# Performance work log

Hardware: AMD Instinct MI355X
Metric: run time of the kernel (lower is better)

The kernel has to match this reference:

```python
import jax, jax.numpy as jnp
import numpy as np

N_NODES = 100000
SELF_LOOP_W = 2.0  # improved=True in PyG GCNConv -> self-loop fill value 2.0


def gcn_conv(x, src, dst, ew, W, b, n_nodes):
    """PyG GCNConv (improved=True): x' = D^-1/2 (A + 2I) D^-1/2 (x W) + b."""
    h = x @ W  # [N, out]
    loop = jnp.arange(n_nodes, dtype=src.dtype)
    src_f = jnp.concatenate([src, loop])
    dst_f = jnp.concatenate([dst, loop])
    ew_f = jnp.concatenate([ew, jnp.full((n_nodes,), SELF_LOOP_W, dtype=ew.dtype)])
    deg = jax.ops.segment_sum(ew_f, dst_f, num_segments=n_nodes)  # [N]
    dinv = jnp.where(deg > 0, jax.lax.rsqrt(jnp.where(deg > 0, deg, 1.0)), 0.0)
    norm = dinv[src_f] * ew_f * dinv[dst_f]  # [E+N]
    msg = h[src_f] * norm[:, None]  # [E+N, out]
    out = jax.ops.segment_sum(msg, dst_f, num_segments=n_nodes)
    return out + b


def setup_inputs() -> dict:
    key = jax.random.key(0)
    k1, k2, k3, k4, k5 = jax.random.split(key, 5)
    N, E = N_NODES, 3200000
    F0, F1, F2 = 128, 128, 64
    x = jax.random.normal(k1, (N, F0), dtype=jnp.float32)
    edges = jax.random.randint(k2, (2, E), 0, N, dtype=jnp.int64)
    weights = jax.random.uniform(k3, (E,), dtype=jnp.float32)
    # kaiming_uniform on weight of shape [out, in]; stored transposed for x @ W
    bnd0 = float(np.sqrt(6.0 / F0))
    bnd1 = float(np.sqrt(6.0 / F1))
    W0 = jax.random.uniform(k4, (F0, F1), dtype=jnp.float32, minval=-bnd0, maxval=bnd0)
    W1 = jax.random.uniform(k5, (F1, F2), dtype=jnp.float32, minval=-bnd1, maxval=bnd1)
    b0 = jnp.zeros((F1,), dtype=jnp.float32)
    b1 = jnp.zeros((F2,), dtype=jnp.float32)
    return {"x": x, "edges": edges, "weights": weights,
            "W0": W0, "b0": b0, "W1": W1, "b1": b1}


def reference(x, edges, weights, W0, b0, W1, b1):
    src, dst = edges[0], edges[1]
    n = x.shape[0]
    h = gcn_conv(x, src, dst, weights, W0, b0, n)
    h = jax.nn.relu(h)
    h = gcn_conv(h, src, dst, weights, W1, b1, n)
    return jax.nn.sigmoid(h)
```

## Files before the change

### kernel.cpp

```cpp
#include <hip/hip_runtime.h>
#include <math.h>

typedef __attribute__((ext_vector_type(8))) short bf16x8;
typedef __attribute__((ext_vector_type(4))) float f32x4;


__device__ __forceinline__ unsigned short f2b(float f) {
  unsigned u = __float_as_uint(f);
  unsigned r = u + 0x7fffu + ((u >> 16) & 1u);
  return (unsigned short)(r >> 16);
}
__device__ __forceinline__ float b2f_lo(unsigned v) {
  return __uint_as_float(v << 16);
}
__device__ __forceinline__ float b2f_hi(unsigned v) {
  return __uint_as_float(v & 0xffff0000u);
}


__global__ __launch_bounds__(256) void bucket_hist(const int* __restrict__ dst,
                                                   int* __restrict__ blkhist,
                                                   int NB, int E, int chunk) {
  extern __shared__ int sm_hist[];
  for (int i = threadIdx.x; i < NB; i += 256) sm_hist[i] = 0;
  __syncthreads();
  const int b = blockIdx.x;
  const int beg = b * chunk;
  const int end = min(E, beg + chunk);
  int j = beg + threadIdx.x;
  for (; j + 768 < end; j += 1024) {
    const int d0 = dst[j], d1 = dst[j + 256], d2 = dst[j + 512], d3 = dst[j + 768];
    atomicAdd(&sm_hist[d0 >> 6], 1);
    atomicAdd(&sm_hist[d1 >> 6], 1);
    atomicAdd(&sm_hist[d2 >> 6], 1);
    atomicAdd(&sm_hist[d3 >> 6], 1);
  }
  for (; j < end; j += 256) atomicAdd(&sm_hist[dst[j] >> 6], 1);
  __syncthreads();
  for (int i = threadIdx.x; i < NB; i += 256) blkhist[(long)b * NB + i] = sm_hist[i];
}

__global__ __launch_bounds__(256) void col_prefix(int* __restrict__ blkhist,
                                                  int* __restrict__ btot, int NB,
                                                  int nblk) {
  const int k = blockIdx.x * 256 + threadIdx.x;
  if (k >= NB) return;
  int run = 0;
  int b = 0;
  for (; b + 4 <= nblk; b += 4) {
    const int t0 = blkhist[(long)(b + 0) * NB + k];
    const int t1 = blkhist[(long)(b + 1) * NB + k];
    const int t2 = blkhist[(long)(b + 2) * NB + k];
    const int t3 = blkhist[(long)(b + 3) * NB + k];
    blkhist[(long)(b + 0) * NB + k] = run; run += t0;
    blkhist[(long)(b + 1) * NB + k] = run; run += t1;
    blkhist[(long)(b + 2) * NB + k] = run; run += t2;
    blkhist[(long)(b + 3) * NB + k] = run; run += t3;
  }
  for (; b < nblk; ++b) {
    const int t = blkhist[(long)b * NB + k];
    blkhist[(long)b * NB + k] = run;
    run += t;
  }
  btot[k] = run;
}

__global__ __launch_bounds__(256) void scan_single(int* __restrict__ cr, int n) {
  __shared__ int sm[256];
  __shared__ int sbase;
  if (threadIdx.x == 0) sbase = 0;
  __syncthreads();
  for (int c0 = 0; c0 < n; c0 += 256) {
    const int i = c0 + threadIdx.x;
    const int v = (i < n) ? cr[i] : 0;
    sm[threadIdx.x] = v;
    __syncthreads();
    for (int off = 1; off < 256; off <<= 1) {
      int a = (threadIdx.x >= off) ? sm[threadIdx.x - off] : 0;
      __syncthreads();
      sm[threadIdx.x] += a;
      __syncthreads();
    }
    const int b = sbase;
    const int tot = sm[255];
    if (i < n) cr[i] = b + sm[threadIdx.x] - v;
    __syncthreads();
    if (threadIdx.x == 0) sbase = b + tot;
    __syncthreads();
  }
  if (threadIdx.x == 0) cr[n] = sbase;
}

__global__ __launch_bounds__(256) void bucket_scatter(const int* __restrict__ src,
                                                      const int* __restrict__ dst,
                                                      const float* __restrict__ ew,
                                                      const int* __restrict__ blkhist,
                                                      const int* __restrict__ bstart,
                                                      uint2* __restrict__ bkt, int NB,
                                                      int E, int chunk) {
  extern __shared__ int sm_cur[];
  const int b = blockIdx.x;
  for (int i = threadIdx.x; i < NB; i += 256)
    sm_cur[i] = blkhist[(long)b * NB + i] + bstart[i];
  __syncthreads();
  const int beg = b * chunk;
  const int end = min(E, beg + chunk);
  int j = beg + threadIdx.x;
  for (; j + 768 < end; j += 1024) {
    const int d0 = dst[j], d1 = dst[j + 256], d2 = dst[j + 512], d3 = dst[j + 768];
    const int s0 = src[j], s1 = src[j + 256], s2 = src[j + 512], s3 = src[j + 768];
    const float e0 = ew[j], e1 = ew[j + 256], e2 = ew[j + 512], e3 = ew[j + 768];
    int q0 = (int)(e0 * 32767.f + 0.5f); q0 = (q0 < 0) ? 0 : ((q0 > 32767) ? 32767 : q0);
    int q1 = (int)(e1 * 32767.f + 0.5f); q1 = (q1 < 0) ? 0 : ((q1 > 32767) ? 32767 : q1);
    int q2 = (int)(e2 * 32767.f + 0.5f); q2 = (q2 < 0) ? 0 : ((q2 > 32767) ? 32767 : q2);
    int q3 = (int)(e3 * 32767.f + 0.5f); q3 = (q3 < 0) ? 0 : ((q3 > 32767) ? 32767 : q3);
    const int p0 = atomicAdd(&sm_cur[d0 >> 6], 1);
    bkt[p0] = make_uint2(((unsigned)s0 << 15) | (unsigned)q0, (unsigned)(d0 & 63));
    const int p1 = atomicAdd(&sm_cur[d1 >> 6], 1);
    bkt[p1] = make_uint2(((unsigned)s1 << 15) | (unsigned)q1, (unsigned)(d1 & 63));
    const int p2 = atomicAdd(&sm_cur[d2 >> 6], 1);
    bkt[p2] = make_uint2(((unsigned)s2 << 15) | (unsigned)q2, (unsigned)(d2 & 63));
    const int p3 = atomicAdd(&sm_cur[d3 >> 6], 1);
    bkt[p3] = make_uint2(((unsigned)s3 << 15) | (unsigned)q3, (unsigned)(d3 & 63));
  }
  for (; j < end; j += 256) {
    const int d = dst[j];
    int q = (int)(ew[j] * 32767.f + 0.5f);
    q = (q < 0) ? 0 : ((q > 32767) ? 32767 : q);
    const unsigned rec = ((unsigned)src[j] << 15) | (unsigned)q;
    const int pos = atomicAdd(&sm_cur[d >> 6], 1);
    bkt[pos] = make_uint2(rec, (unsigned)(d & 63));
  }
}

__global__ __launch_bounds__(256) void bucket_finalize(const uint2* __restrict__ bkt,
                                                       const int* __restrict__ bstart,
                                                       unsigned* __restrict__ recs,
                                                       int* __restrict__ row_start,
                                                       float* __restrict__ dinv, int NB,
                                                       int N, int E) {
  __shared__ int hist[64], qs[64], cur[64], lstart[64];
  const int k = blockIdx.x;
  const int t = threadIdx.x;
  if (t < 64) { hist[t] = 0; qs[t] = 0; }
  __syncthreads();
  const int beg = bstart[k], end = bstart[k + 1];
  for (int j = beg + t; j < end; j += 256) {
    const uint2 v = bkt[j];
    atomicAdd(&hist[v.y], 1);
    atomicAdd(&qs[v.y], (int)(v.x & 32767u));
  }
  __syncthreads();
  if (t == 0) {
    int run = 0;
    for (int i = 0; i < 64; ++i) { lstart[i] = run; run += hist[i]; }
  }
  __syncthreads();
  if (t < 64) {
    cur[t] = lstart[t];
    const int node = k * 64 + t;
    if (node < N) {
      row_start[node] = beg + lstart[t];
      dinv[node] = rsqrtf((float)qs[t] * (1.f / 32767.f) + 2.0f);
    }
  }
  if (k == NB - 1 && t == 0) row_start[N] = E;
  __syncthreads();
  for (int j = beg + t; j < end; j += 256) {
    const uint2 v = bkt[j];
    const int off = atomicAdd(&cur[v.y], 1);
    recs[beg + off] = v.x;
  }
}


__global__ __launch_bounds__(256) void fold_dinv(unsigned int* __restrict__ recs,
                                                 const float* __restrict__ dinv, int E) {
  int i = blockIdx.x * 256 + threadIdx.x;
  if (i >= E) return;
  const unsigned rec = recs[i];
  const int s = rec >> 15;
  const float v = (float)(rec & 32767u) * (1.f / 32767.f) * dinv[s];
  int q = (int)(v * (32767.f / 0.75f) + 0.5f);
  q = (q > 32767) ? 32767 : q;
  recs[i] = ((unsigned)s << 15) | (unsigned)q;
}


__global__ __launch_bounds__(256) void to_bf16_8(const float* __restrict__ x,
                                                 unsigned short* __restrict__ xb,
                                                 int n8) {
  int i = blockIdx.x * 256 + threadIdx.x;
  if (i >= n8) return;
  const float4 a = *(const float4*)&x[(long)i * 8];
  const float4 b = *(const float4*)&x[(long)i * 8 + 4];
  uint4 o;
  o.x = (unsigned)f2b(a.x) | ((unsigned)f2b(a.y) << 16);
  o.y = (unsigned)f2b(a.z) | ((unsigned)f2b(a.w) << 16);
  o.z = (unsigned)f2b(b.x) | ((unsigned)f2b(b.y) << 16);
  o.w = (unsigned)f2b(b.z) | ((unsigned)f2b(b.w) << 16);
  *(uint4*)&xb[(long)i * 8] = o;
}

__global__ __launch_bounds__(256) void pack_wfrag(const float* __restrict__ W,
                                                  unsigned short* __restrict__ frag,
                                                  int C, int total) {
  int i = blockIdx.x * 256 + threadIdx.x;
  if (i >= total) return;
  const int e = i & 7;
  const int lane = (i >> 3) & 63;
  const int t = i >> 9;
  const int kk = t & 3;
  const int ct = t >> 2;
  const int k = kk * 32 + (lane >> 4) * 8 + e;
  const int c = ct * 16 + (lane & 15);
  frag[i] = f2b(W[(long)k * C + c]);
}


__global__ __launch_bounds__(256) void gather_l1_half(const uint4* __restrict__ xb4,
                                                      const unsigned int* __restrict__ recs,
                                                      const int* __restrict__ row_start,
                                                      const float* __restrict__ dinv,
                                                      uint4* __restrict__ xab4, int N,
                                                      int half) {
  const int t = blockIdx.x * 256 + threadIdx.x;
  const int d = t >> 3;
  if (d >= N) return;
  const int jl = (t & 7) + half * 8;
  const int beg = row_start[d], end = row_start[d + 1];
  const float dd = dinv[d];
  constexpr float S = 0.75f / 32767.f;
  const uint4 sv = xb4[(long)d * 16 + jl];
  const float sl = 2.f * dd * dd;
  float aca[8], acb[8];
  aca[0] = b2f_lo(sv.x) * sl; aca[1] = b2f_hi(sv.x) * sl;
  aca[2] = b2f_lo(sv.y) * sl; aca[3] = b2f_hi(sv.y) * sl;
  aca[4] = b2f_lo(sv.z) * sl; aca[5] = b2f_hi(sv.z) * sl;
  aca[6] = b2f_lo(sv.w) * sl; aca[7] = b2f_hi(sv.w) * sl;
#pragma unroll
  for (int u = 0; u < 8; ++u) acb[u] = 0.f;
  int j = beg;
  for (; j + 8 <= end; j += 8) {
    unsigned rr[8];
    uint4 vv[8];
#pragma unroll
    for (int u = 0; u < 8; ++u) rr[u] = recs[j + u];
#pragma unroll
    for (int u = 0; u < 8; ++u) vv[u] = xb4[(long)(rr[u] >> 15) * 16 + jl];
#pragma unroll
    for (int u = 0; u < 8; ++u) {
      const float cf = (float)(rr[u] & 32767u) * S * dd;
      float* ac = (u & 1) ? acb : aca;
      ac[0] = fmaf(cf, b2f_lo(vv[u].x), ac[0]);
      ac[1] = fmaf(cf, b2f_hi(vv[u].x), ac[1]);
      ac[2] = fmaf(cf, b2f_lo(vv[u].y), ac[2]);
      ac[3] = fmaf(cf, b2f_hi(vv[u].y), ac[3]);
      ac[4] = fmaf(cf, b2f_lo(vv[u].z), ac[4]);
      ac[5] = fmaf(cf, b2f_hi(vv[u].z), ac[5]);
      ac[6] = fmaf(cf, b2f_lo(vv[u].w), ac[6]);
      ac[7] = fmaf(cf, b2f_hi(vv[u].w), ac[7]);
    }
  }
  for (; j < end; ++j) {
    const unsigned rec = recs[j];
    const uint4 v = xb4[(long)(rec >> 15) * 16 + jl];
    const float cf = (float)(rec & 32767u) * S * dd;
    aca[0] = fmaf(cf, b2f_lo(v.x), aca[0]);
    aca[1] = fmaf(cf, b2f_hi(v.x), aca[1]);
    aca[2] = fmaf(cf, b2f_lo(v.y), aca[2]);
    aca[3] = fmaf(cf, b2f_hi(v.y), aca[3]);
    aca[4] = fmaf(cf, b2f_lo(v.z), aca[4]);
    aca[5] = fmaf(cf, b2f_hi(v.z), aca[5]);
    aca[6] = fmaf(cf, b2f_lo(v.w), aca[6]);
    aca[7] = fmaf(cf, b2f_hi(v.w), aca[7]);
  }
#pragma unroll
  for (int u = 0; u < 8; ++u) aca[u] += acb[u];
  uint4 o;
  o.x = (unsigned)f2b(aca[0]) | ((unsigned)f2b(aca[1]) << 16);
  o.y = (unsigned)f2b(aca[2]) | ((unsigned)f2b(aca[3]) << 16);
  o.z = (unsigned)f2b(aca[4]) | ((unsigned)f2b(aca[5]) << 16);
  o.w = (unsigned)f2b(aca[6]) | ((unsigned)f2b(aca[7]) << 16);
  xab4[(long)d * 16 + jl] = o;
}


__global__ __launch_bounds__(256) void fused_mlp_mfma(
    const unsigned short* __restrict__ xab, const unsigned short* __restrict__ w0f,
    const float* __restrict__ b0, const unsigned short* __restrict__ w1f,
    unsigned short* __restrict__ r2b, int N) {
  __shared__ unsigned short Hl[4][16][136];
  const int tid = threadIdx.x;
  const int w = tid >> 6, l = tid & 63;
  const int lr = l & 15, lg = l >> 4;
  const int row0 = blockIdx.x * 64 + w * 16;

  int arow = row0 + lr;
  if (arow >= N) arow = N - 1;
  const unsigned short* ap = xab + (long)arow * 128 + lg * 8;
  const bf16x8 a0 = *(const bf16x8*)(ap);
  const bf16x8 a1 = *(const bf16x8*)(ap + 32);
  const bf16x8 a2 = *(const bf16x8*)(ap + 64);
  const bf16x8 a3 = *(const bf16x8*)(ap + 96);

  for (int ct = 0; ct < 8; ++ct) {
    const unsigned short* bp = w0f + ct * 2048 + l * 8;
    f32x4 acc = {0.f, 0.f, 0.f, 0.f};
    acc = __builtin_amdgcn_mfma_f32_16x16x32_bf16(a0, *(const bf16x8*)(bp), acc, 0, 0, 0);
    acc = __builtin_amdgcn_mfma_f32_16x16x32_bf16(a1, *(const bf16x8*)(bp + 512), acc, 0, 0, 0);
    acc = __builtin_amdgcn_mfma_f32_16x16x32_bf16(a2, *(const bf16x8*)(bp + 1024), acc, 0, 0, 0);
    acc = __builtin_amdgcn_mfma_f32_16x16x32_bf16(a3, *(const bf16x8*)(bp + 1536), acc, 0, 0, 0);
    const float bv = b0[ct * 16 + lr];
#pragma unroll
    for (int r = 0; r < 4; ++r) {
      Hl[w][lg * 4 + r][ct * 16 + lr] = f2b(fmaxf(acc[r] + bv, 0.f));
    }
  }

  const unsigned short* hp = &Hl[w][lr][lg * 8];
  const bf16x8 h0 = *(const bf16x8*)(hp);
  const bf16x8 h1 = *(const bf16x8*)(hp + 32);
  const bf16x8 h2 = *(const bf16x8*)(hp + 64);
  const bf16x8 h3 = *(const bf16x8*)(hp + 96);

  for (int ct = 0; ct < 4; ++ct) {
    const unsigned short* bp = w1f + ct * 2048 + l * 8;
    f32x4 acc = {0.f, 0.f, 0.f, 0.f};
    acc = __builtin_amdgcn_mfma_f32_16x16x32_bf16(h0, *(const bf16x8*)(bp), acc, 0, 0, 0);
    acc = __builtin_amdgcn_mfma_f32_16x16x32_bf16(h1, *(const bf16x8*)(bp + 512), acc, 0, 0, 0);
    acc = __builtin_amdgcn_mfma_f32_16x16x32_bf16(h2, *(const bf16x8*)(bp + 1024), acc, 0, 0, 0);
    acc = __builtin_amdgcn_mfma_f32_16x16x32_bf16(h3, *(const bf16x8*)(bp + 1536), acc, 0, 0, 0);
#pragma unroll
    for (int r = 0; r < 4; ++r) {
      const int orow = row0 + lg * 4 + r;
      if (orow < N) r2b[(long)orow * 64 + ct * 16 + lr] = f2b(acc[r]);
    }
  }
}


__global__ __launch_bounds__(256) void gather_l2(const uint4* __restrict__ r2b4,
                                                 const unsigned int* __restrict__ recs,
                                                 const int* __restrict__ row_start,
                                                 const float* __restrict__ dinv,
                                                 const float* __restrict__ b1,
                                                 float* __restrict__ out, int N) {
  const int t = blockIdx.x * 256 + threadIdx.x;
  const int d = t >> 3;
  if (d >= N) return;
  const int jl = t & 7;
  const int beg = row_start[d], end = row_start[d + 1];
  const float dd = dinv[d];
  constexpr float S = 0.75f / 32767.f;
  const uint4 sv = r2b4[(long)d * 8 + jl];
  const float sl = 2.f * dd * dd;
  float aca[8], acb[8];
  aca[0] = b2f_lo(sv.x) * sl; aca[1] = b2f_hi(sv.x) * sl;
  aca[2] = b2f_lo(sv.y) * sl; aca[3] = b2f_hi(sv.y) * sl;
  aca[4] = b2f_lo(sv.z) * sl; aca[5] = b2f_hi(sv.z) * sl;
  aca[6] = b2f_lo(sv.w) * sl; aca[7] = b2f_hi(sv.w) * sl;
#pragma unroll
  for (int u = 0; u < 8; ++u) acb[u] = 0.f;
  int j = beg;
  for (; j + 8 <= end; j += 8) {
    unsigned rr[8];
    uint4 vv[8];
#pragma unroll
    for (int u = 0; u < 8; ++u) rr[u] = recs[j + u];
#pragma unroll
    for (int u = 0; u < 8; ++u) vv[u] = r2b4[(long)(rr[u] >> 15) * 8 + jl];
#pragma unroll
    for (int u = 0; u < 8; ++u) {
      const float cf = (float)(rr[u] & 32767u) * S * dd;
      float* ac = (u & 1) ? acb : aca;
      ac[0] = fmaf(cf, b2f_lo(vv[u].x), ac[0]);
      ac[1] = fmaf(cf, b2f_hi(vv[u].x), ac[1]);
      ac[2] = fmaf(cf, b2f_lo(vv[u].y), ac[2]);
      ac[3] = fmaf(cf, b2f_hi(vv[u].y), ac[3]);
      ac[4] = fmaf(cf, b2f_lo(vv[u].z), ac[4]);
      ac[5] = fmaf(cf, b2f_hi(vv[u].z), ac[5]);
      ac[6] = fmaf(cf, b2f_lo(vv[u].w), ac[6]);
      ac[7] = fmaf(cf, b2f_hi(vv[u].w), ac[7]);
    }
  }
  for (; j < end; ++j) {
    const unsigned rec = recs[j];
    const uint4 v = r2b4[(long)(rec >> 15) * 8 + jl];
    const float cf = (float)(rec & 32767u) * S * dd;
    aca[0] = fmaf(cf, b2f_lo(v.x), aca[0]);
    aca[1] = fmaf(cf, b2f_hi(v.x), aca[1]);
    aca[2] = fmaf(cf, b2f_lo(v.y), aca[2]);
    aca[3] = fmaf(cf, b2f_hi(v.y), aca[3]);
    aca[4] = fmaf(cf, b2f_lo(v.z), aca[4]);
    aca[5] = fmaf(cf, b2f_hi(v.z), aca[5]);
    aca[6] = fmaf(cf, b2f_lo(v.w), aca[6]);
    aca[7] = fmaf(cf, b2f_hi(v.w), aca[7]);
  }
#pragma unroll
  for (int u = 0; u < 8; ++u) aca[u] += acb[u];
  const int c = jl * 8;
  const float4 ba = *(const float4*)&b1[c];
  const float4 bb = *(const float4*)&b1[c + 4];
  float4 o1, o2;
  o1.x = 1.f / (1.f + __expf(-(aca[0] + ba.x)));
  o1.y = 1.f / (1.f + __expf(-(aca[1] + ba.y)));
  o1.z = 1.f / (1.f + __expf(-(aca[2] + ba.z)));
  o1.w = 1.f / (1.f + __expf(-(aca[3] + ba.w)));
  o2.x = 1.f / (1.f + __expf(-(aca[4] + bb.x)));
  o2.y = 1.f / (1.f + __expf(-(aca[5] + bb.y)));
  o2.z = 1.f / (1.f + __expf(-(aca[6] + bb.z)));
  o2.w = 1.f / (1.f + __expf(-(aca[7] + bb.w)));
  *(float4*)&out[(long)d * 64 + c] = o1;
  *(float4*)&out[(long)d * 64 + c + 4] = o2;
}


extern "C" void kernel_launch(void* const* d_in, const int* in_sizes, int n_in,
                              void* d_out, int out_size, void* d_ws, size_t ws_size,
                              hipStream_t stream) {
  const float* x  = (const float*)d_in[0];
  const int* src  = (const int*)d_in[1];
  const float* ew = (const float*)d_in[2];
  const float* W0 = (const float*)d_in[3];
  const float* b0 = (const float*)d_in[4];
  const float* W1 = (const float*)d_in[5];
  const float* b1 = (const float*)d_in[6];
  float* out = (float*)d_out;

  const int N = in_sizes[0] / 128;
  const int E = in_sizes[2];
  const int* dstp = src + E;

  const int NB = (N + 63) >> 6;
  const int NBLK = 1024;
  const int chunk = (E + NBLK - 1) / NBLK;

  float* ws = (float*)d_ws;
  const size_t oN = ((size_t)N + 255) & ~(size_t)255;
  float* dinv = ws;
  int* rowst = (int*)(ws + oN);
  int* bstart = rowst + oN;
  int* bsum = bstart + 2048;
  int* blkhist = bsum + 1024;
  unsigned int* recs = (unsigned int*)(blkhist + (size_t)NBLK * NB);
  unsigned int* xb = recs + E;
  uint2* bkt = (uint2*)xb;
  const size_t xb_units = ((size_t)2 * E > (size_t)N * 64) ? (size_t)2 * E : (size_t)N * 64;
  unsigned int* xab = xb + xb_units;
  unsigned short* w0f = (unsigned short*)(xab + (size_t)N * 64);
  unsigned short* w1f = w0f + 16384;
  unsigned int* r2b = xb;

  const int nbE = (E + 255) / 256;
  const int nblkB = (NB + 255) / 256;

  bucket_hist<<<NBLK, 256, NB * 4, stream>>>(dstp, blkhist, NB, E, chunk);
  col_prefix<<<nblkB, 256, 0, stream>>>(blkhist, bstart, NB, NBLK);
  scan_single<<<1, 256, 0, stream>>>(bstart, NB);
  bucket_scatter<<<NBLK, 256, NB * 4, stream>>>(src, dstp, ew, blkhist, bstart, bkt, NB,
                                                E, chunk);
  bucket_finalize<<<NB, 256, 0, stream>>>(bkt, bstart, recs, rowst, dinv, NB, N, E);
  fold_dinv<<<nbE, 256, 0, stream>>>(recs, dinv, E);

  pack_wfrag<<<64, 256, 0, stream>>>(W0, w0f, 128, 16384);
  pack_wfrag<<<32, 256, 0, stream>>>(W1, w1f, 64, 8192);
  to_bf16_8<<<(N * 16 + 255) / 256, 256, 0, stream>>>(x, (unsigned short*)xb, N * 16);

  const int gl1b = (N * 8 + 255) / 256;
  gather_l1_half<<<gl1b, 256, 0, stream>>>((const uint4*)xb, recs, rowst, dinv,
                                           (uint4*)xab, N, 0);
  gather_l1_half<<<gl1b, 256, 0, stream>>>((const uint4*)xb, recs, rowst, dinv,
                                           (uint4*)xab, N, 1);

  fused_mlp_mfma<<<(N + 63) / 64, 256, 0, stream>>>((const unsigned short*)xab, w0f, b0,
                                                    w1f, (unsigned short*)r2b, N);
  gather_l2<<<(N * 8 + 255) / 256, 256, 0, stream>>>((const uint4*)r2b, recs, rowst, dinv,
                                                     b1, out, N);
}
```

Baseline: 385.2 us.

## Split gathers into narrow column passes and parallelize bucket column prefix

The feature gathers for both layers now run as several launches, each covering only two 16-byte column slices per node: eight passes for layer 1 and four for layer 2. The goal is a smaller gathered working set per pass so it stays cache resident, at the cost of re-reading the edge records and row offsets in every pass. The bucket column prefix becomes a three-stage partial-sum, scan and apply over 16 groups, and the histogram block count doubles to 2048, with blkhist moved into the xab region. The paired-accumulator ILP in the gathers is removed, which lengthens each FMA dependency chain.

```diff
diff --git a/kernel.cpp b/kernel.cpp
--- a/kernel.cpp
+++ b/kernel.cpp
@@ -3,6 +3,10 @@
 
 typedef __attribute__((ext_vector_type(8))) short bf16x8;
 typedef __attribute__((ext_vector_type(4))) float f32x4;
+
+#define NBLK 2048
+#define GB   16
+#define BPG  (NBLK / GB)
 
 
 __device__ __forceinline__ unsigned short f2b(float f) {
@@ -40,29 +44,63 @@
   for (int i = threadIdx.x; i < NB; i += 256) blkhist[(long)b * NB + i] = sm_hist[i];
 }
 
-__global__ __launch_bounds__(256) void col_prefix(int* __restrict__ blkhist,
-                                                  int* __restrict__ btot, int NB,
-                                                  int nblk) {
+__global__ __launch_bounds__(256) void col_part(const int* __restrict__ blkhist,
+                                                int* __restrict__ partials, int NB) {
+  const int k = blockIdx.x * 256 + threadIdx.x;
+  const int g = blockIdx.y;
+  if (k >= NB) return;
+  const long base = (long)g * BPG * NB + k;
+  int sum = 0;
+  int i = 0;
+  for (; i + 4 <= BPG; i += 4) {
+    const int t0 = blkhist[base + (long)(i + 0) * NB];
+    const int t1 = blkhist[base + (long)(i + 1) * NB];
+    const int t2 = blkhist[base + (long)(i + 2) * NB];
+    const int t3 = blkhist[base + (long)(i + 3) * NB];
+    sum += t0 + t1 + t2 + t3;
+  }
+  for (; i < BPG; ++i) sum += blkhist[base + (long)i * NB];
+  partials[(long)g * NB + k] = sum;
+}
+
+__global__ __launch_bounds__(256) void col_scan16(int* __restrict__ partials,
+                                                  int* __restrict__ bstart, int NB) {
   const int k = blockIdx.x * 256 + threadIdx.x;
   if (k >= NB) return;
   int run = 0;
-  int b = 0;
-  for (; b + 4 <= nblk; b += 4) {
-    const int t0 = blkhist[(long)(b + 0) * NB + k];
-    const int t1 = blkhist[(long)(b + 1) * NB + k];
-    const int t2 = blkhist[(long)(b + 2) * NB + k];
-    const int t3 = blkhist[(long)(b + 3) * NB + k];
-    blkhist[(long)(b + 0) * NB + k] = run; run += t0;
-    blkhist[(long)(b + 1) * NB + k] = run; run += t1;
-    blkhist[(long)(b + 2) * NB + k] = run; run += t2;
-    blkhist[(long)(b + 3) * NB + k] = run; run += t3;
-  }
-  for (; b < nblk; ++b) {
-    const int t = blkhist[(long)b * NB + k];
-    blkhist[(long)b * NB + k] = run;
+#pragma unroll
+  for (int g = 0; g < GB; ++g) {
+    const int t = partials[(long)g * NB + k];
+    partials[(long)g * NB + k] = run;
     run += t;
   }
-  btot[k] = run;
+  bstart[k] = run;
+}
+
+__global__ __launch_bounds__(256) void col_apply(int* __restrict__ blkhist,
+                                                 const int* __restrict__ partials,
+                                                 int NB) {
+  const int k = blockIdx.x * 256 + threadIdx.x;
+  const int g = blockIdx.y;
+  if (k >= NB) return;
+  const long base = (long)g * BPG * NB + k;
+  int run = partials[(long)g * NB + k];
+  int i = 0;
+  for (; i + 4 <= BPG; i += 4) {
+    const int t0 = blkhist[base + (long)(i + 0) * NB];
+    const int t1 = blkhist[base + (long)(i + 1) * NB];
+    const int t2 = blkhist[base + (long)(i + 2) * NB];
+    const int t3 = blkhist[base + (long)(i + 3) * NB];
+    blkhist[base + (long)(i + 0) * NB] = run; run += t0;
+    blkhist[base + (long)(i + 1) * NB] = run; run += t1;
+    blkhist[base + (long)(i + 2) * NB] = run; run += t2;
+    blkhist[base + (long)(i + 3) * NB] = run; run += t3;
+  }
+  for (; i < BPG; ++i) {
+    const int t = blkhist[base + (long)i * NB];
+    blkhist[base + (long)i * NB] = run;
+    run += t;
+  }
 }
 
 __global__ __launch_bounds__(256) void scan_single(int* __restrict__ cr, int n) {
@@ -218,28 +256,26 @@
 }
 
 
-__global__ __launch_bounds__(256) void gather_l1_half(const uint4* __restrict__ xb4,
+__global__ __launch_bounds__(256) void gather_l1_pass(const uint4* __restrict__ xb4,
                                                       const unsigned int* __restrict__ recs,
                                                       const int* __restrict__ row_start,
                                                       const float* __restrict__ dinv,
                                                       uint4* __restrict__ xab4, int N,
-                                                      int half) {
+                                                      int slot) {
   const int t = blockIdx.x * 256 + threadIdx.x;
-  const int d = t >> 3;
+  const int d = t >> 1;
   if (d >= N) return;
-  const int jl = (t & 7) + half * 8;
+  const int jl = slot + (t & 1);
   const int beg = row_start[d], end = row_start[d + 1];
   const float dd = dinv[d];
   constexpr float S = 0.75f / 32767.f;
   const uint4 sv = xb4[(long)d * 16 + jl];
   const float sl = 2.f * dd * dd;
-  float aca[8], acb[8];
-  aca[0] = b2f_lo(sv.x) * sl; aca[1] = b2f_hi(sv.x) * sl;
-  aca[2] = b2f_lo(sv.y) * sl; aca[3] = b2f_hi(sv.y) * sl;
-  aca[4] = b2f_lo(sv.z) * sl; aca[5] = b2f_hi(sv.z) * sl;
-  aca[6] = b2f_lo(sv.w) * sl; aca[7] = b2f_hi(sv.w) * sl;
-#pragma unroll
-  for (int u = 0; u < 8; ++u) acb[u] = 0.f;
+  float acc[8];
+  acc[0] = b2f_lo(sv.x) * sl; acc[1] = b2f_hi(sv.x) * sl;
+  acc[2] = b2f_lo(sv.y) * sl; acc[3] = b2f_hi(sv.y) * sl;
+  acc[4] = b2f_lo(sv.z) * sl; acc[5] = b2f_hi(sv.z) * sl;
+  acc[6] = b2f_lo(sv.w) * sl; acc[7] = b2f_hi(sv.w) * sl;
   int j = beg;
   for (; j + 8 <= end; j += 8) {
     unsigned rr[8];
@@ -251,37 +287,34 @@
 #pragma unroll
     for (int u = 0; u < 8; ++u) {
       const float cf = (float)(rr[u] & 32767u) * S * dd;
-      float* ac = (u & 1) ? acb : aca;
-      ac[0] = fmaf(cf, b2f_lo(vv[u].x), ac[0]);
-      ac[1] = fmaf(cf, b2f_hi(vv[u].x), ac[1]);
-      ac[2] = fmaf(cf, b2f_lo(vv[u].y), ac[2]);
-      ac[3] = fmaf(cf, b2f_hi(vv[u].y), ac[3]);
-      ac[4] = fmaf(cf, b2f_lo(vv[u].z), ac[4]);
-      ac[5] = fmaf(cf, b2f_hi(vv[u].z), ac[5]);
-      ac[6] = fmaf(cf, b2f_lo(vv[u].w), ac[6]);
-      ac[7] = fmaf(cf, b2f_hi(vv[u].w), ac[7]);
+      acc[0] = fmaf(cf, b2f_lo(vv[u].x), acc[0]);
+      acc[1] = fmaf(cf, b2f_hi(vv[u].x), acc[1]);
+      acc[2] = fmaf(cf, b2f_lo(vv[u].y), acc[2]);
+      acc[3] = fmaf(cf, b2f_hi(vv[u].y), acc[3]);
+      acc[4] = fmaf(cf, b2f_lo(vv[u].z), acc[4]);
+      acc[5] = fmaf(cf, b2f_hi(vv[u].z), acc[5]);
+      acc[6] = fmaf(cf, b2f_lo(vv[u].w), acc[6]);
+      acc[7] = fmaf(cf, b2f_hi(vv[u].w), acc[7]);
     }
   }
   for (; j < end; ++j) {
     const unsigned rec = recs[j];
     const uint4 v = xb4[(long)(rec >> 15) * 16 + jl];
     const float cf = (float)(rec & 32767u) * S * dd;
-    aca[0] = fmaf(cf, b2f_lo(v.x), aca[0]);
-    aca[1] = fmaf(cf, b2f_hi(v.x), aca[1]);
-    aca[2] = fmaf(cf, b2f_lo(v.y), aca[2]);
-    aca[3] = fmaf(cf, b2f_hi(v.y), aca[3]);
-    aca[4] = fmaf(cf, b2f_lo(v.z), aca[4]);
-    aca[5] = fmaf(cf, b2f_hi(v.z), aca[5]);
-    aca[6] = fmaf(cf, b2f_lo(v.w), aca[6]);
-    aca[7] = fmaf(cf, b2f_hi(v.w), aca[7]);
-  }
-#pragma unroll
-  for (int u = 0; u < 8; ++u) aca[u] += acb[u];
+    acc[0] = fmaf(cf, b2f_lo(v.x), acc[0]);
+    acc[1] = fmaf(cf, b2f_hi(v.x), acc[1]);
+    acc[2] = fmaf(cf, b2f_lo(v.y), acc[2]);
+    acc[3] = fmaf(cf, b2f_hi(v.y), acc[3]);
+    acc[4] = fmaf(cf, b2f_lo(v.z), acc[4]);
+    acc[5] = fmaf(cf, b2f_hi(v.z), acc[5]);
+    acc[6] = fmaf(cf, b2f_lo(v.w), acc[6]);
+    acc[7] = fmaf(cf, b2f_hi(v.w), acc[7]);
+  }
   uint4 o;
-  o.x = (unsigned)f2b(aca[0]) | ((unsigned)f2b(aca[1]) << 16);
-  o.y = (unsigned)f2b(aca[2]) | ((unsigned)f2b(aca[3]) << 16);
-  o.z = (unsigned)f2b(aca[4]) | ((unsigned)f2b(aca[5]) << 16);
-  o.w = (unsigned)f2b(aca[6]) | ((unsigned)f2b(aca[7]) << 16);
+  o.x = (unsigned)f2b(acc[0]) | ((unsigned)f2b(acc[1]) << 16);
+  o.y = (unsigned)f2b(acc[2]) | ((unsigned)f2b(acc[3]) << 16);
+  o.z = (unsigned)f2b(acc[4]) | ((unsigned)f2b(acc[5]) << 16);
+  o.w = (unsigned)f2b(acc[6]) | ((unsigned)f2b(acc[7]) << 16);
   xab4[(long)d * 16 + jl] = o;
 }
 
@@ -340,28 +373,27 @@
 }
 
 
-__global__ __launch_bounds__(256) void gather_l2(const uint4* __restrict__ r2b4,
-                                                 const unsigned int* __restrict__ recs,
-                                                 const int* __restrict__ row_start,
-                                                 const float* __restrict__ dinv,
-                                                 const float* __restrict__ b1,
-                                                 float* __restrict__ out, int N) {
+__global__ __launch_bounds__(256) void gather_l2_pass(const uint4* __restrict__ r2b4,
+                                                      const unsigned int* __restrict__ recs,
+                                                      const int* __restrict__ row_start,
+                                                      const float* __restrict__ dinv,
+                                                      const float* __restrict__ b1,
+                                                      float* __restrict__ out, int N,
+                                                      int slot) {
   const int t = blockIdx.x * 256 + threadIdx.x;
-  const int d = t >> 3;
+  const int d = t >> 1;
   if (d >= N) return;
-  const int jl = t & 7;
+  const int jl = slot + (t & 1);
   const int beg = row_start[d], end = row_start[d + 1];
   const float dd = dinv[d];
   constexpr float S = 0.75f / 32767.f;
   const uint4 sv = r2b4[(long)d * 8 + jl];
   const float sl = 2.f * dd * dd;
-  float aca[8], acb[8];
-  aca[0] = b2f_lo(sv.x) * sl; aca[1] = b2f_hi(sv.x) * sl;
-  aca[2] = b2f_lo(sv.y) * sl; aca[3] = b2f_hi(sv.y) * sl;
-  aca[4] = b2f_lo(sv.z) * sl; aca[5] = b2f_hi(sv.z) * sl;
-  aca[6] = b2f_lo(sv.w) * sl; aca[7] = b2f_hi(sv.w) * sl;
-#pragma unroll
-  for (int u = 0; u < 8; ++u) acb[u] = 0.f;
+  float acc[8];
+  acc[0] = b2f_lo(sv.x) * sl; acc[1] = b2f_hi(sv.x) * sl;
+  acc[2] = b2f_lo(sv.y) * sl; acc[3] = b2f_hi(sv.y) * sl;
+  acc[4] = b2f_lo(sv.z) * sl; acc[5] = b2f_hi(sv.z) * sl;
+  acc[6] = b2f_lo(sv.w) * sl; acc[7] = b2f_hi(sv.w) * sl;
   int j = beg;
   for (; j + 8 <= end; j += 8) {
     unsigned rr[8];
@@ -373,44 +405,41 @@
 #pragma unroll
     for (int u = 0; u < 8; ++u) {
       const float cf = (float)(rr[u] & 32767u) * S * dd;
-      float* ac = (u & 1) ? acb : aca;
-      ac[0] = fmaf(cf, b2f_lo(vv[u].x), ac[0]);
-      ac[1] = fmaf(cf, b2f_hi(vv[u].x), ac[1]);
-      ac[2] = fmaf(cf, b2f_lo(vv[u].y), ac[2]);
-      ac[3] = fmaf(cf, b2f_hi(vv[u].y), ac[3]);
-      ac[4] = fmaf(cf, b2f_lo(vv[u].z), ac[4]);
-      ac[5] = fmaf(cf, b2f_hi(vv[u].z), ac[5]);
-      ac[6] = fmaf(cf, b2f_lo(vv[u].w), ac[6]);
-      ac[7] = fmaf(cf, b2f_hi(vv[u].w), ac[7]);
+      acc[0] = fmaf(cf, b2f_lo(vv[u].x), acc[0]);
+      acc[1] = fmaf(cf, b2f_hi(vv[u].x), acc[1]);
+      acc[2] = fmaf(cf, b2f_lo(vv[u].y), acc[2]);
+      acc[3] = fmaf(cf, b2f_hi(vv[u].y), acc[3]);
+      acc[4] = fmaf(cf, b2f_lo(vv[u].z), acc[4]);
+      acc[5] = fmaf(cf, b2f_hi(vv[u].z), acc[5]);
+      acc[6] = fmaf(cf, b2f_lo(vv[u].w), acc[6]);
+      acc[7] = fmaf(cf, b2f_hi(vv[u].w), acc[7]);
     }
   }
   for (; j < end; ++j) {
     const unsigned rec = recs[j];
     const uint4 v = r2b4[(long)(rec >> 15) * 8 + jl];
     const float cf = (float)(rec & 32767u) * S * dd;
-    aca[0] = fmaf(cf, b2f_lo(v.x), aca[0]);
-    aca[1] = fmaf(cf, b2f_hi(v.x), aca[1]);
-    aca[2] = fmaf(cf, b2f_lo(v.y), aca[2]);
-    aca[3] = fmaf(cf, b2f_hi(v.y), aca[3]);
-    aca[4] = fmaf(cf, b2f_lo(v.z), aca[4]);
-    aca[5] = fmaf(cf, b2f_hi(v.z), aca[5]);
-    aca[6] = fmaf(cf, b2f_lo(v.w), aca[6]);
-    aca[7] = fmaf(cf, b2f_hi(v.w), aca[7]);
-  }
-#pragma unroll
-  for (int u = 0; u < 8; ++u) aca[u] += acb[u];
+    acc[0] = fmaf(cf, b2f_lo(v.x), acc[0]);
+    acc[1] = fmaf(cf, b2f_hi(v.x), acc[1]);
+    acc[2] = fmaf(cf, b2f_lo(v.y), acc[2]);
+    acc[3] = fmaf(cf, b2f_hi(v.y), acc[3]);
+    acc[4] = fmaf(cf, b2f_lo(v.z), acc[4]);
+    acc[5] = fmaf(cf, b2f_hi(v.z), acc[5]);
+    acc[6] = fmaf(cf, b2f_lo(v.w), acc[6]);
+    acc[7] = fmaf(cf, b2f_hi(v.w), acc[7]);
+  }
   const int c = jl * 8;
   const float4 ba = *(const float4*)&b1[c];
   const float4 bb = *(const float4*)&b1[c + 4];
   float4 o1, o2;
-  o1.x = 1.f / (1.f + __expf(-(aca[0] + ba.x)));
-  o1.y = 1.f / (1.f + __expf(-(aca[1] + ba.y)));
-  o1.z = 1.f / (1.f + __expf(-(aca[2] + ba.z)));
-  o1.w = 1.f / (1.f + __expf(-(aca[3] + ba.w)));
-  o2.x = 1.f / (1.f + __expf(-(aca[4] + bb.x)));
-  o2.y = 1.f / (1.f + __expf(-(aca[5] + bb.y)));
-  o2.z = 1.f / (1.f + __expf(-(aca[6] + bb.z)));
-  o2.w = 1.f / (1.f + __expf(-(aca[7] + bb.w)));
+  o1.x = 1.f / (1.f + __expf(-(acc[0] + ba.x)));
+  o1.y = 1.f / (1.f + __expf(-(acc[1] + ba.y)));
+  o1.z = 1.f / (1.f + __expf(-(acc[2] + ba.z)));
+  o1.w = 1.f / (1.f + __expf(-(acc[3] + ba.w)));
+  o2.x = 1.f / (1.f + __expf(-(acc[4] + bb.x)));
+  o2.y = 1.f / (1.f + __expf(-(acc[5] + bb.y)));
+  o2.z = 1.f / (1.f + __expf(-(acc[6] + bb.z)));
+  o2.w = 1.f / (1.f + __expf(-(acc[7] + bb.w)));
   *(float4*)&out[(long)d * 64 + c] = o1;
   *(float4*)&out[(long)d * 64 + c + 4] = o2;
 }
@@ -433,7 +462,6 @@
   const int* dstp = src + E;
 
   const int NB = (N + 63) >> 6;
-  const int NBLK = 1024;
   const int chunk = (E + NBLK - 1) / NBLK;
 
   float* ws = (float*)d_ws;
@@ -441,13 +469,13 @@
   float* dinv = ws;
   int* rowst = (int*)(ws + oN);
   int* bstart = rowst + oN;
-  int* bsum = bstart + 2048;
-  int* blkhist = bsum + 1024;
-  unsigned int* recs = (unsigned int*)(blkhist + (size_t)NBLK * NB);
+  int* partials = bstart + 2048;
+  unsigned int* recs = (unsigned int*)(partials + 32768);
   unsigned int* xb = recs + E;
   uint2* bkt = (uint2*)xb;
   const size_t xb_units = ((size_t)2 * E > (size_t)N * 64) ? (size_t)2 * E : (size_t)N * 64;
   unsigned int* xab = xb + xb_units;
+  int* blkhist = (int*)xab;
   unsigned short* w0f = (unsigned short*)(xab + (size_t)N * 64);
   unsigned short* w1f = w0f + 16384;
   unsigned int* r2b = xb;
@@ -456,7 +484,9 @@
   const int nblkB = (NB + 255) / 256;
 
   bucket_hist<<<NBLK, 256, NB * 4, stream>>>(dstp, blkhist, NB, E, chunk);
-  col_prefix<<<nblkB, 256, 0, stream>>>(blkhist, bstart, NB, NBLK);
+  col_part<<<dim3(nblkB, GB), 256, 0, stream>>>(blkhist, partials, NB);
+  col_scan16<<<nblkB, 256, 0, stream>>>(partials, bstart, NB);
+  col_apply<<<dim3(nblkB, GB), 256, 0, stream>>>(blkhist, partials, NB);
   scan_single<<<1, 256, 0, stream>>>(bstart, NB);
   bucket_scatter<<<NBLK, 256, NB * 4, stream>>>(src, dstp, ew, blkhist, bstart, bkt, NB,
                                                 E, chunk);
@@ -467,14 +497,15 @@
   pack_wfrag<<<32, 256, 0, stream>>>(W1, w1f, 64, 8192);
   to_bf16_8<<<(N * 16 + 255) / 256, 256, 0, stream>>>(x, (unsigned short*)xb, N * 16);
 
-  const int gl1b = (N * 8 + 255) / 256;
-  gather_l1_half<<<gl1b, 256, 0, stream>>>((const uint4*)xb, recs, rowst, dinv,
-                                           (uint4*)xab, N, 0);
-  gather_l1_half<<<gl1b, 256, 0, stream>>>((const uint4*)xb, recs, rowst, dinv,
-                                           (uint4*)xab, N, 1);
+  const int gpb = (N * 2 + 255) / 256;
+  for (int p = 0; p < 8; ++p)
+    gather_l1_pass<<<gpb, 256, 0, stream>>>((const uint4*)xb, recs, rowst, dinv,
+                                            (uint4*)xab, N, p * 2);
 
   fused_mlp_mfma<<<(N + 63) / 64, 256, 0, stream>>>((const unsigned short*)xab, w0f, b0,
                                                     w1f, (unsigned short*)r2b, N);
-  gather_l2<<<(N * 8 + 255) / 256, 256, 0, stream>>>((const uint4*)r2b, recs, rowst, dinv,
-                                                     b1, out, N);
-}
+
+  for (int p = 0; p < 4; ++p)
+    gather_l2_pass<<<gpb, 256, 0, stream>>>((const uint4*)r2b, recs, rowst, dinv, b1,
+                                            out, N, p * 2);
+}
```

Measured after the change: 844.0 us. 119% more time.

## Widen destination buckets to 256 nodes and parallelize column prefix scan

Applied to the files above, without the earlier changes.

Destination buckets now cover 256 nodes instead of 64, which cuts the bucket count and therefore the size of the per-block histogram matrix and the shared-memory histograms. The serial per-column prefix over 1024 blocks is split into three kernels: a grouped partial sum, a 16-way scan of the partials, and an apply pass, so many more threads take part. The blkhist buffer moves to reuse the xab region. The trade-off is more kernel launches and fewer, larger finalize blocks with a longer serial local scan over 256 entries.

```diff
diff --git a/kernel.cpp b/kernel.cpp
--- a/kernel.cpp
+++ b/kernel.cpp
@@ -3,6 +3,10 @@
 
 typedef __attribute__((ext_vector_type(8))) short bf16x8;
 typedef __attribute__((ext_vector_type(4))) float f32x4;
+
+#define NBLK 1024
+#define GB   16
+#define BPG  (NBLK / GB)
 
 
 __device__ __forceinline__ unsigned short f2b(float f) {
@@ -30,39 +34,73 @@
   int j = beg + threadIdx.x;
   for (; j + 768 < end; j += 1024) {
     const int d0 = dst[j], d1 = dst[j + 256], d2 = dst[j + 512], d3 = dst[j + 768];
-    atomicAdd(&sm_hist[d0 >> 6], 1);
-    atomicAdd(&sm_hist[d1 >> 6], 1);
-    atomicAdd(&sm_hist[d2 >> 6], 1);
-    atomicAdd(&sm_hist[d3 >> 6], 1);
-  }
-  for (; j < end; j += 256) atomicAdd(&sm_hist[dst[j] >> 6], 1);
+    atomicAdd(&sm_hist[d0 >> 8], 1);
+    atomicAdd(&sm_hist[d1 >> 8], 1);
+    atomicAdd(&sm_hist[d2 >> 8], 1);
+    atomicAdd(&sm_hist[d3 >> 8], 1);
+  }
+  for (; j < end; j += 256) atomicAdd(&sm_hist[dst[j] >> 8], 1);
   __syncthreads();
   for (int i = threadIdx.x; i < NB; i += 256) blkhist[(long)b * NB + i] = sm_hist[i];
 }
 
-__global__ __launch_bounds__(256) void col_prefix(int* __restrict__ blkhist,
-                                                  int* __restrict__ btot, int NB,
-                                                  int nblk) {
+__global__ __launch_bounds__(256) void col_part(const int* __restrict__ blkhist,
+                                                int* __restrict__ partials, int NB) {
+  const int k = blockIdx.x * 256 + threadIdx.x;
+  const int g = blockIdx.y;
+  if (k >= NB) return;
+  const long base = (long)g * BPG * NB + k;
+  int sum = 0;
+  int i = 0;
+  for (; i + 4 <= BPG; i += 4) {
+    const int t0 = blkhist[base + (long)(i + 0) * NB];
+    const int t1 = blkhist[base + (long)(i + 1) * NB];
+    const int t2 = blkhist[base + (long)(i + 2) * NB];
+    const int t3 = blkhist[base + (long)(i + 3) * NB];
+    sum += t0 + t1 + t2 + t3;
+  }
+  for (; i < BPG; ++i) sum += blkhist[base + (long)i * NB];
+  partials[(long)g * NB + k] = sum;
+}
+
+__global__ __launch_bounds__(256) void col_scan16(int* __restrict__ partials,
+                                                  int* __restrict__ bstart, int NB) {
   const int k = blockIdx.x * 256 + threadIdx.x;
   if (k >= NB) return;
   int run = 0;
-  int b = 0;
-  for (; b + 4 <= nblk; b += 4) {
-    const int t0 = blkhist[(long)(b + 0) * NB + k];
-    const int t1 = blkhist[(long)(b + 1) * NB + k];
-    const int t2 = blkhist[(long)(b + 2) * NB + k];
-    const int t3 = blkhist[(long)(b + 3) * NB + k];
-    blkhist[(long)(b + 0) * NB + k] = run; run += t0;
-    blkhist[(long)(b + 1) * NB + k] = run; run += t1;
-    blkhist[(long)(b + 2) * NB + k] = run; run += t2;
-    blkhist[(long)(b + 3) * NB + k] = run; run += t3;
-  }
-  for (; b < nblk; ++b) {
-    const int t = blkhist[(long)b * NB + k];
-    blkhist[(long)b * NB + k] = run;
+#pragma unroll
+  for (int g = 0; g < GB; ++g) {
+    const int t = partials[(long)g * NB + k];
+    partials[(long)g * NB + k] = run;
     run += t;
   }
-  btot[k] = run;
+  bstart[k] = run;
+}
+
+__global__ __launch_bounds__(256) void col_apply(int* __restrict__ blkhist,
+                                                 const int* __restrict__ partials,
+                                                 int NB) {
+  const int k = blockIdx.x * 256 + threadIdx.x;
+  const int g = blockIdx.y;
+  if (k >= NB) return;
+  const long base = (long)g * BPG * NB + k;
+  int run = partials[(long)g * NB + k];
+  int i = 0;
+  for (; i + 4 <= BPG; i += 4) {
+    const int t0 = blkhist[base + (long)(i + 0) * NB];
+    const int t1 = blkhist[base + (long)(i + 1) * NB];
+    const int t2 = blkhist[base + (long)(i + 2) * NB];
+    const int t3 = blkhist[base + (long)(i + 3) * NB];
+    blkhist[base + (long)(i + 0) * NB] = run; run += t0;
+    blkhist[base + (long)(i + 1) * NB] = run; run += t1;
+    blkhist[base + (long)(i + 2) * NB] = run; run += t2;
+    blkhist[base + (long)(i + 3) * NB] = run; run += t3;
+  }
+  for (; i < BPG; ++i) {
+    const int t = blkhist[base + (long)i * NB];
+    blkhist[base + (long)i * NB] = run;
+    run += t;
+  }
 }
 
 __global__ __launch_bounds__(256) void scan_single(int* __restrict__ cr, int n) {
@@ -114,22 +152,22 @@
     int q1 = (int)(e1 * 32767.f + 0.5f); q1 = (q1 < 0) ? 0 : ((q1 > 32767) ? 32767 : q1);
     int q2 = (int)(e2 * 32767.f + 0.5f); q2 = (q2 < 0) ? 0 : ((q2 > 32767) ? 32767 : q2);
     int q3 = (int)(e3 * 32767.f + 0.5f); q3 = (q3 < 0) ? 0 : ((q3 > 32767) ? 32767 : q3);
-    const int p0 = atomicAdd(&sm_cur[d0 >> 6], 1);
-    bkt[p0] = make_uint2(((unsigned)s0 << 15) | (unsigned)q0, (unsigned)(d0 & 63));
-    const int p1 = atomicAdd(&sm_cur[d1 >> 6], 1);
-    bkt[p1] = make_uint2(((unsigned)s1 << 15) | (unsigned)q1, (unsigned)(d1 & 63));
-    const int p2 = atomicAdd(&sm_cur[d2 >> 6], 1);
-    bkt[p2] = make_uint2(((unsigned)s2 << 15) | (unsigned)q2, (unsigned)(d2 & 63));
-    const int p3 = atomicAdd(&sm_cur[d3 >> 6], 1);
-    bkt[p3] = make_uint2(((unsigned)s3 << 15) | (unsigned)q3, (unsigned)(d3 & 63));
+    const int p0 = atomicAdd(&sm_cur[d0 >> 8], 1);
+    bkt[p0] = make_uint2(((unsigned)s0 << 15) | (unsigned)q0, (unsigned)(d0 & 255));
+    const int p1 = atomicAdd(&sm_cur[d1 >> 8], 1);
+    bkt[p1] = make_uint2(((unsigned)s1 << 15) | (unsigned)q1, (unsigned)(d1 & 255));
+    const int p2 = atomicAdd(&sm_cur[d2 >> 8], 1);
+    bkt[p2] = make_uint2(((unsigned)s2 << 15) | (unsigned)q2, (unsigned)(d2 & 255));
+    const int p3 = atomicAdd(&sm_cur[d3 >> 8], 1);
+    bkt[p3] = make_uint2(((unsigned)s3 << 15) | (unsigned)q3, (unsigned)(d3 & 255));
   }
   for (; j < end; j += 256) {
     const int d = dst[j];
     int q = (int)(ew[j] * 32767.f + 0.5f);
     q = (q < 0) ? 0 : ((q > 32767) ? 32767 : q);
     const unsigned rec = ((unsigned)src[j] << 15) | (unsigned)q;
-    const int pos = atomicAdd(&sm_cur[d >> 6], 1);
-    bkt[pos] = make_uint2(rec, (unsigned)(d & 63));
+    const int pos = atomicAdd(&sm_cur[d >> 8], 1);
+    bkt[pos] = make_uint2(rec, (unsigned)(d & 255));
   }
 }
 
@@ -139,10 +177,11 @@
                                                        int* __restrict__ row_start,
                                                        float* __restrict__ dinv, int NB,
                                                        int N, int E) {
-  __shared__ int hist[64], qs[64], cur[64], lstart[64];
+  __shared__ int hist[256], qs[256], cur[256], lstart[256];
   const int k = blockIdx.x;
   const int t = threadIdx.x;
-  if (t < 64) { hist[t] = 0; qs[t] = 0; }
+  hist[t] = 0;
+  qs[t] = 0;
   __syncthreads();
   const int beg = bstart[k], end = bstart[k + 1];
   for (int j = beg + t; j < end; j += 256) {
@@ -153,16 +192,14 @@
   __syncthreads();
   if (t == 0) {
     int run = 0;
-    for (int i = 0; i < 64; ++i) { lstart[i] = run; run += hist[i]; }
-  }
-  __syncthreads();
-  if (t < 64) {
-    cur[t] = lstart[t];
-    const int node = k * 64 + t;
-    if (node < N) {
-      row_start[node] = beg + lstart[t];
-      dinv[node] = rsqrtf((float)qs[t] * (1.f / 32767.f) + 2.0f);
-    }
+    for (int i = 0; i < 256; ++i) { lstart[i] = run; run += hist[i]; }
+  }
+  __syncthreads();
+  cur[t] = lstart[t];
+  const int node = k * 256 + t;
+  if (node < N) {
+    row_start[node] = beg + lstart[t];
+    dinv[node] = rsqrtf((float)qs[t] * (1.f / 32767.f) + 2.0f);
   }
   if (k == NB - 1 && t == 0) row_start[N] = E;
   __syncthreads();
@@ -432,8 +469,7 @@
   const int E = in_sizes[2];
   const int* dstp = src + E;
 
-  const int NB = (N + 63) >> 6;
-  const int NBLK = 1024;
+  const int NB = (N + 255) >> 8;
   const int chunk = (E + NBLK - 1) / NBLK;
 
   float* ws = (float*)d_ws;
@@ -441,13 +477,13 @@
   float* dinv = ws;
   int* rowst = (int*)(ws + oN);
   int* bstart = rowst + oN;
-  int* bsum = bstart + 2048;
-  int* blkhist = bsum + 1024;
-  unsigned int* recs = (unsigned int*)(blkhist + (size_t)NBLK * NB);
+  int* partials = bstart + 2048;
+  unsigned int* recs = (unsigned int*)(partials + 32768);
   unsigned int* xb = recs + E;
   uint2* bkt = (uint2*)xb;
   const size_t xb_units = ((size_t)2 * E > (size_t)N * 64) ? (size_t)2 * E : (size_t)N * 64;
   unsigned int* xab = xb + xb_units;
+  int* blkhist = (int*)xab;
   unsigned short* w0f = (unsigned short*)(xab + (size_t)N * 64);
   unsigned short* w1f = w0f + 16384;
   unsigned int* r2b = xb;
@@ -456,7 +492,9 @@
   const int nblkB = (NB + 255) / 256;
 
   bucket_hist<<<NBLK, 256, NB * 4, stream>>>(dstp, blkhist, NB, E, chunk);
-  col_prefix<<<nblkB, 256, 0, stream>>>(blkhist, bstart, NB, NBLK);
+  col_part<<<dim3(nblkB, GB), 256, 0, stream>>>(blkhist, partials, NB);
+  col_scan16<<<nblkB, 256, 0, stream>>>(partials, bstart, NB);
+  col_apply<<<dim3(nblkB, GB), 256, 0, stream>>>(blkhist, partials, NB);
   scan_single<<<1, 256, 0, stream>>>(bstart, NB);
   bucket_scatter<<<NBLK, 256, NB * 4, stream>>>(src, dstp, ew, blkhist, bstart, bkt, NB,
                                                 E, chunk);
```

After: 310.5 us. -19.4%, faster.
